# Performance work log

Hardware: AMD Instinct MI355X
Metric: run time of the kernel (lower is better)

## Reference

```python
import jax, jax.numpy as jnp
import numpy as np

IMG = 224
RADIUS_CUTS, AZIMUTH_CUTS = 16, 64
N_RADIUS, N_AZIMUTH = 25, 16          # kr1*kr2 = 25, ka^2 = 16
N_R = RADIUS_CUTS * N_RADIUS          # 400 sampled radii
N_A = AZIMUTH_CUTS * N_AZIMUTH        # 1024 sampled azimuths
EMBED_DIM = 96
KR, KA = 5, 4


def sample_grid(dist, H, W):
    """Per-batch polar sampling coordinates for the spherical distortion model.
    dist: (B, 4) polynomial distortion coefficients (module does dist.transpose(1,0)).
    Returns grid (B, N_R, N_A, 2) in grid_sample convention (x=width coord first),
    and theta_max (B,).
    """
    B = dist.shape[0]
    cf = 0.2 + dist.T                      # (4, B), positive odd-poly coefficients
    c = cf[:, :, None]                     # (4, B, 1) for broadcasting
    theta_max = jnp.full((B,), jnp.pi / 2, dtype=dist.dtype)

    def poly(t):                           # odd polynomial r(theta), t: (B, n)
        t2 = t * t
        return t * (c[0] + t2 * (c[1] + t2 * (c[2] + t2 * c[3])))

    # midpoint theta samples in (0, theta_max)
    theta = theta_max[:, None] * (jnp.arange(N_R, dtype=dist.dtype) + 0.5) / N_R  # (B, N_R)
    r = poly(theta) / poly(theta_max[:, None]) * (H * 0.5)                        # (B, N_R) pixels from center

    phi = (2.0 * jnp.pi) * (jnp.arange(N_A, dtype=dist.dtype) + 0.5) / N_A        # (N_A,)
    xc = r[:, :, None] * jnp.cos(phi)      # (B, N_R, N_A)
    yc = r[:, :, None] * jnp.sin(phi)
    # module: out = cat((yc/(W//2), xc/(H//2)), dim=3)
    grid = jnp.stack([yc / (W // 2), xc / (H // 2)], axis=-1)
    return grid, theta_max


def grid_sample_bilinear(img, grid):
    """torch.nn.functional.grid_sample, bilinear, align_corners=True, zeros padding.
    img: (B,C,H,W), grid: (B,Ho,Wo,2) with grid[...,0]=x (width), grid[...,1]=y (height).
    """
    B, C, H, W = img.shape
    gx = (grid[..., 0] + 1.0) * 0.5 * (W - 1)   # align_corners=True mapping
    gy = (grid[..., 1] + 1.0) * 0.5 * (H - 1)
    x0 = jnp.floor(gx); y0 = jnp.floor(gy)
    wx1 = gx - x0; wx0 = 1.0 - wx1
    wy1 = gy - y0; wy0 = 1.0 - wy1

    def corner(xi, yi, w):
        valid = (xi >= 0) & (xi <= W - 1) & (yi >= 0) & (yi <= H - 1)
        xc_ = jnp.clip(xi, 0, W - 1).astype(jnp.int32)
        yc_ = jnp.clip(yi, 0, H - 1).astype(jnp.int32)
        v = jax.vmap(lambda im, yy, xx: im[:, yy, xx])(img, yc_, xc_)  # (B,C,Ho,Wo)
        return v * (w * valid)[:, None, :, :]

    return (corner(x0, y0, wx0 * wy0) + corner(x0 + 1, y0, wx1 * wy0)
            + corner(x0, y0 + 1, wx0 * wy1) + corner(x0 + 1, y0 + 1, wx1 * wy1))


def conv2d(x, w, b, stride):
    y = jax.lax.conv_general_dilated(x, w, window_strides=stride, padding='VALID',
                                     dimension_numbers=('NCHW', 'OIHW', 'NCHW'))
    return y + b[None, :, None, None]


def setup_inputs() -> dict:
    key = jax.random.key(0)
    k = jax.random.split(key, 6)
    x = jax.random.uniform(k[0], (32, 3, IMG, IMG), dtype=jnp.float32)
    dist = jax.random.uniform(k[1], (32, 4), dtype=jnp.float32)
    w1 = jax.random.normal(k[2], (EMBED_DIM, 3, KR, KA), dtype=jnp.float32) * 0.05
    b1 = jnp.zeros((EMBED_DIM,), dtype=jnp.float32)
    w2 = jax.random.normal(k[3], (EMBED_DIM, EMBED_DIM, KR, KA), dtype=jnp.float32) * 0.05
    b2 = jnp.zeros((EMBED_DIM,), dtype=jnp.float32)
    return {"x": x, "dist": dist, "w1": w1, "b1": b1, "w2": w2, "b2": b2}


def reference(x, dist, w1, b1, w2, b2):
    B, C, H, W = x.shape
    grid, theta_max = sample_grid(dist, H, W)          # (B,400,1024,2)
    sampled = grid_sample_bilinear(x, grid)            # (B,3,400,1024)
    t = conv2d(sampled, w1, b1, (KR, KA))              # (B,96,80,256)
    t = conv2d(t, w2, b2, (KR, KA))                    # (B,96,16,64)
    t = t.reshape(B, EMBED_DIM, -1).transpose(0, 2, 1) # (B,1024,96)
    return (t, theta_max)
```

## Files before the change

kernel.cpp:

```cpp
#include <hip/hip_runtime.h>
#include <hip/hip_bf16.h>
#include <math.h>

#define NBATCH 32
#define IMGSZ  224
#define NR     400
#define NA     1024
#define ED     96
#define SROW   266

typedef __attribute__((ext_vector_type(8))) __bf16 bf16x8;
typedef __attribute__((ext_vector_type(8), aligned(8))) __bf16 bf16x8u;
typedef __attribute__((ext_vector_type(4), aligned(8))) __bf16 bf16x4a;
typedef __attribute__((ext_vector_type(4))) __bf16 bf16x4;
typedef __attribute__((ext_vector_type(4))) float f32x4;

union frag_u { struct { bf16x4a lo, hi; } p; bf16x8 v; };


#define PACK_N   (NBATCH*IMGSZ*IMGSZ)
#define PACK_N4  (PACK_N/4)
#define PACK_B   ((PACK_N4 + 255)/256)
#define PREP_N   (ED*ED*20 + 12*64*8 + NBATCH*NR + NA + NBATCH)
#define PREP_B   ((PREP_N + 255)/256)

__global__ __launch_bounds__(256)
void prep_pack_kernel(const float* __restrict__ x,
                      const float* __restrict__ dist,
                      const float* __restrict__ w1,
                      const float* __restrict__ w2,
                      __bf16* __restrict__ xp,
                      float* __restrict__ rtab,
                      float* __restrict__ costab,
                      float* __restrict__ sintab,
                      __bf16* __restrict__ w2f,
                      __bf16* __restrict__ w1f,
                      float* __restrict__ theta_out) {
    const float PI = 3.14159265358979323846f;
    const float SC = 223.0f / 224.0f;
    int bid = blockIdx.x;

    if (bid < PACK_B) {
        int i4 = bid*256 + threadIdx.x;
        if (i4 >= PACK_N4) return;
        int idx = i4 * 4;
        int b  = idx / (IMGSZ*IMGSZ);
        int px = idx - b*(IMGSZ*IMGSZ);
        const float* p = x + (size_t)b*3*IMGSZ*IMGSZ + px;
        f32x4 cr = *(const f32x4*)(p);
        f32x4 cg = *(const f32x4*)(p + IMGSZ*IMGSZ);
        f32x4 cb = *(const f32x4*)(p + 2*IMGSZ*IMGSZ);
        bf16x8 o0, o1;
        o0[0] = (__bf16)cr[0]; o0[1] = (__bf16)cg[0]; o0[2] = (__bf16)cb[0]; o0[3] = (__bf16)0.0f;
        o0[4] = (__bf16)cr[1]; o0[5] = (__bf16)cg[1]; o0[6] = (__bf16)cb[1]; o0[7] = (__bf16)0.0f;
        o1[0] = (__bf16)cr[2]; o1[1] = (__bf16)cg[2]; o1[2] = (__bf16)cb[2]; o1[3] = (__bf16)0.0f;
        o1[4] = (__bf16)cr[3]; o1[5] = (__bf16)cg[3]; o1[6] = (__bf16)cb[3]; o1[7] = (__bf16)0.0f;
        *(bf16x8*)(xp + (size_t)idx*4)     = o0;
        *(bf16x8*)(xp + (size_t)idx*4 + 8) = o1;
        return;
    }

    int idx = (bid - PACK_B)*256 + threadIdx.x;
    if (idx < ED*ED*20) {
        int j    = idx & 7;
        int lane = (idx >> 3) & 63;
        int grp  = idx >> 9;
        int nt   = grp % 6;
        int t    = grp / 6;
        int icb  = t % 3;
        int p    = t / 3;
        int sw   = (((p & 3) + icb) & 1) * 4;
        int oc = nt*16 + (lane & 15);
        int ic = icb*32 + (lane >> 4)*8 + (j ^ sw);
        w2f[idx] = (__bf16)w2[((size_t)(oc*ED + ic)*5 + (p >> 2))*4 + (p & 3)];
    } else if (idx < ED*ED*20 + 12*64*8) {
        int i2   = idx - ED*ED*20;
        int j    = i2 & 7;
        int lane = (i2 >> 3) & 63;
        int grp  = i2 >> 9;
        int ks = grp / 6, ot = grp % 6;
        int oc = ot*16 + (lane & 15);
        int k  = ks*32 + (lane >> 4)*8 + j;
        w1f[i2] = (k < 60) ? (__bf16)w1[oc*60 + k] : (__bf16)0.0f;
    } else if (idx < ED*ED*20 + 12*64*8 + NBATCH*NR) {
        int i2 = idx - ED*ED*20 - 12*64*8;
        int b = i2 / NR, i = i2 % NR;
        float c0 = 0.2f + dist[b*4+0];
        float c1 = 0.2f + dist[b*4+1];
        float c2 = 0.2f + dist[b*4+2];
        float c3 = 0.2f + dist[b*4+3];
        float tmax = 0.5f * PI;
        float t  = tmax * ((float)i + 0.5f) / (float)NR;
        float t2 = t * t;
        float pt = t * (c0 + t2*(c1 + t2*(c2 + t2*c3)));
        float tm2 = tmax * tmax;
        float pm = tmax * (c0 + tm2*(c1 + tm2*(c2 + tm2*c3)));
        rtab[i2] = pt / pm * (0.5f * (float)IMGSZ);
    } else if (idx < ED*ED*20 + 12*64*8 + NBATCH*NR + NA) {
        int j = idx - ED*ED*20 - 12*64*8 - NBATCH*NR;
        float phi = 2.0f * PI * ((float)j + 0.5f) / (float)NA;
        costab[j] = cosf(phi) * SC;
        sintab[j] = sinf(phi) * SC;
    } else if (idx < PREP_N) {
        theta_out[idx - (ED*ED*20 + 12*64*8 + NBATCH*NR + NA)] = 0.5f * PI;
    }
}

__global__ __launch_bounds__(256, 4)
void mega_kernel(const __bf16* __restrict__ xp,
                 const __bf16* __restrict__ w1f_g,
                 const __bf16* __restrict__ w2f,
                 const float* __restrict__ b1,
                 const float* __restrict__ b2,
                 const float* __restrict__ rtab,
                 const float* __restrict__ costab,
                 const float* __restrict__ sintab,
                 float* __restrict__ out) {
    __shared__ __attribute__((aligned(16))) char smem[32576];
    __bf16* s_samp = (__bf16*)smem;
    __bf16* t1f    = (__bf16*)(smem + 8000);
    __bf16* s_w1f  = (__bf16*)(smem + 20288);
    float*  red    = (float*)smem;

    int tid = threadIdx.x;
    int bid = blockIdx.x;
    int r2h = bid & 7;
    int aq  = (bid >> 3) & 3;
    int b   = bid >> 5;
    int wave = tid >> 6, lane = tid & 63, l15 = lane & 15, quad = lane >> 4;

    #pragma unroll
    for (int i = 0; i < 3; ++i)
        *(bf16x8*)(s_w1f + i*2048 + tid*8) = *(const bf16x8*)(w1f_g + i*2048 + tid*8);

    int az = aq*256 + tid;
    float sn = sintab[az];
    float cs = costab[az];
    const __bf16* xpb = xp + (size_t)b*IMGSZ*IMGSZ*4;
    const float* rb;

    auto sample = [&](int kr) {
        #pragma unroll
        for (int q = 0; q < 5; ++q) {
            float r  = rb[kr*5 + q];
            float gx = fmaf(r, sn, 111.5f);
            float gy = fmaf(r, cs, 111.5f);
            float x0f = floorf(gx), y0f = floorf(gy);
            float wx1 = gx - x0f, wx0 = 1.0f - wx1;
            float wy1 = gy - y0f, wy0 = 1.0f - wy1;
            int ix = (int)x0f, iy = (int)y0f;
            ix = min(max(ix, 0), IMGSZ-2);
            iy = min(max(iy, 0), IMGSZ-2);
            const __bf16* img = xpb + ((size_t)iy*IMGSZ + ix)*4;
            bf16x8u p0 = *(const bf16x8u*)img;
            bf16x8u p1 = *(const bf16x8u*)(img + IMGSZ*4);
            float w00 = wy0*wx0, w01 = wy0*wx1, w10 = wy1*wx0, w11 = wy1*wx1;
            #pragma unroll
            for (int c = 0; c < 3; ++c) {
                float v = w00*(float)p0[c] + w01*(float)p0[4+c]
                        + w10*(float)p1[c] + w11*(float)p1[4+c];
                s_samp[(c*5 + q)*SROW + tid] = (__bf16)v;
            }
        }
    };

    #pragma unroll 1
    for (int u = 0; u < 2; ++u) {
        int r2 = r2h*2 + u;
        rb = rtab + b*NR + r2*25;

        if (u) __syncthreads();

        f32x4 acc2[6];
        #pragma unroll
        for (int nt = 0; nt < 6; ++nt) acc2[nt] = (f32x4){0.f,0.f,0.f,0.f};

        sample(0);

        for (int kr = 0; kr < 5; ++kr) {
            __syncthreads();

            int colb = (wave*16 + l15)*4;
            f32x4 acc1[6];
            #pragma unroll
            for (int ot = 0; ot < 6; ++ot) acc1[ot] = (f32x4){0.f,0.f,0.f,0.f};

            frag_u fa, fb;
            fa.p.lo = *(const bf16x4a*)&s_samp[(quad*2    )*SROW + colb];
            fa.p.hi = *(const bf16x4a*)&s_samp[(quad*2 + 1)*SROW + colb];
            fb.p.lo = *(const bf16x4a*)&s_samp[(8 + quad*2)*SROW + colb];
            if (quad == 3) fb.p.hi = (bf16x4a){};
            else           fb.p.hi = *(const bf16x4a*)&s_samp[(9 + quad*2)*SROW + colb];

            #pragma unroll
            for (int ot = 0; ot < 6; ++ot) {
                bf16x8 wf0 = *(const bf16x8*)(s_w1f + (ot     )*512 + lane*8);
                bf16x8 wf1 = *(const bf16x8*)(s_w1f + (6 + ot )*512 + lane*8);
                acc1[ot] = __builtin_amdgcn_mfma_f32_16x16x32_bf16(wf0, fa.v, acc1[ot], 0, 0, 0);
                acc1[ot] = __builtin_amdgcn_mfma_f32_16x16x32_bf16(wf1, fb.v, acc1[ot], 0, 0, 0);
            }

            int pixel = wave*16 + l15;
            int a2l = pixel >> 2, ka = pixel & 3;
            #pragma unroll
            for (int ot = 0; ot < 6; ++ot) {
                f32x4 v = acc1[ot] + *(const f32x4*)(b1 + ot*16 + quad*4);
                bf16x4a wv;
                wv[0] = (__bf16)v[0]; wv[1] = (__bf16)v[1];
                wv[2] = (__bf16)v[2]; wv[3] = (__bf16)v[3];
                int icbase = ot*16 + quad*4;
                int kk = ka*3 + (icbase >> 5);
                int qT = (icbase >> 3) & 3;
                int jb = (icbase & 7) ^ ((kk & 1)*4);
                *(bf16x4a*)&t1f[((kk*4 + qT)*16 + a2l)*8 + jb] = wv;
            }
            __syncthreads();

            #pragma unroll
            for (int icb = 0; icb < 3; ++icb) {
                int kk = wave*3 + icb;
                int p  = kr*4 + wave;
                bf16x8 af = *(const bf16x8*)&t1f[(kk*64 + lane)*8];
                const __bf16* wp = w2f + (size_t)((p*3 + icb)*6)*512 + lane*8;
                #pragma unroll
                for (int nt = 0; nt < 6; ++nt) {
                    bf16x8 bf = *(const bf16x8*)(wp + nt*512);
                    acc2[nt] = __builtin_amdgcn_mfma_f32_16x16x32_bf16(af, bf, acc2[nt], 0, 0, 0);
                }
            }

            __builtin_amdgcn_sched_barrier(0);

            if (kr < 4) sample(kr + 1);
        }

        __syncthreads();
        if (wave) {
            float* rw = red + (wave - 1)*1568;
            #pragma unroll
            for (int nt = 0; nt < 6; ++nt)
                #pragma unroll
                for (int r = 0; r < 4; ++r)
                    rw[(quad*4 + r)*98 + nt*16 + l15] = acc2[nt][r];
        }
        __syncthreads();
        if (wave == 0) {
            size_t ob = ((size_t)b*1024 + r2*64 + aq*16)*ED;
            #pragma unroll
            for (int nt = 0; nt < 6; ++nt) {
                int oc = nt*16 + l15;
                float bias = b2[oc];
                #pragma unroll
                for (int r = 0; r < 4; ++r) {
                    int row = quad*4 + r;
                    float v = acc2[nt][r] + bias
                            + red[row*98 + oc]
                            + red[1568 + row*98 + oc]
                            + red[3136 + row*98 + oc];
                    out[ob + (size_t)row*ED + oc] = v;
                }
            }
        }
    }
}

extern "C" void kernel_launch(void* const* d_in, const int* in_sizes, int n_in,
                              void* d_out, int out_size, void* d_ws, size_t ws_size,
                              hipStream_t stream) {
    const float* x    = (const float*)d_in[0];
    const float* dist = (const float*)d_in[1];
    const float* w1   = (const float*)d_in[2];
    const float* b1   = (const float*)d_in[3];
    const float* w2   = (const float*)d_in[4];
    const float* b2   = (const float*)d_in[5];
    float* out = (float*)d_out;

    float* rtab   = (float*)d_ws;
    float* costab = rtab + NBATCH*NR;
    float* sintab = costab + NA;
    __bf16* w2f   = (__bf16*)(sintab + NA);
    __bf16* w1f   = w2f + ED*ED*20;
    __bf16* xp    = w1f + 12*64*8;

    float* theta_out = out + (size_t)NBATCH*1024*ED;

    prep_pack_kernel<<<PACK_B + PREP_B, 256, 0, stream>>>(
        x, dist, w1, w2, xp, rtab, costab, sintab, w2f, w1f, theta_out);
    mega_kernel<<<NBATCH*32, 256, 0, stream>>>(
        xp, w1f, w2f, b1, b2, rtab, costab, sintab, out);
}
```

Baseline: 165.0 us.

## Pack image rows with next-row pixels and split mega kernel per radius row

Adds an optional packed image layout in which each pixel holds its own RGB and the RGB of the pixel one row below. A bilinear tap then needs two adjacent 16-byte loads instead of two loads one row apart. This path is selected when the workspace is large enough, and it doubles the packed image size and prep write traffic. Separately, the mega kernel now handles one radius row per block instead of looping over two, doubling the grid to 2048 blocks. That raises parallelism but repeats the per-block w1 staging and sin/cos loads.

```diff
diff --git a/kernel.cpp b/kernel.cpp
--- a/kernel.cpp
+++ b/kernel.cpp
@@ -24,6 +24,7 @@
 #define PREP_N   (ED*ED*20 + 12*64*8 + NBATCH*NR + NA + NBATCH)
 #define PREP_B   ((PREP_N + 255)/256)
 
+template<bool RD>
 __global__ __launch_bounds__(256)
 void prep_pack_kernel(const float* __restrict__ x,
                       const float* __restrict__ dist,
@@ -44,19 +45,41 @@
         int i4 = bid*256 + threadIdx.x;
         if (i4 >= PACK_N4) return;
         int idx = i4 * 4;
-        int b  = idx / (IMGSZ*IMGSZ);
-        int px = idx - b*(IMGSZ*IMGSZ);
-        const float* p = x + (size_t)b*3*IMGSZ*IMGSZ + px;
-        f32x4 cr = *(const f32x4*)(p);
-        f32x4 cg = *(const f32x4*)(p + IMGSZ*IMGSZ);
-        f32x4 cb = *(const f32x4*)(p + 2*IMGSZ*IMGSZ);
-        bf16x8 o0, o1;
-        o0[0] = (__bf16)cr[0]; o0[1] = (__bf16)cg[0]; o0[2] = (__bf16)cb[0]; o0[3] = (__bf16)0.0f;
-        o0[4] = (__bf16)cr[1]; o0[5] = (__bf16)cg[1]; o0[6] = (__bf16)cb[1]; o0[7] = (__bf16)0.0f;
-        o1[0] = (__bf16)cr[2]; o1[1] = (__bf16)cg[2]; o1[2] = (__bf16)cb[2]; o1[3] = (__bf16)0.0f;
-        o1[4] = (__bf16)cr[3]; o1[5] = (__bf16)cg[3]; o1[6] = (__bf16)cb[3]; o1[7] = (__bf16)0.0f;
-        *(bf16x8*)(xp + (size_t)idx*4)     = o0;
-        *(bf16x8*)(xp + (size_t)idx*4 + 8) = o1;
+        int b   = idx / (IMGSZ*IMGSZ);
+        int rem = idx - b*(IMGSZ*IMGSZ);
+        const float* pl = x + (size_t)b*3*IMGSZ*IMGSZ;
+        if constexpr (RD) {
+            int y    = rem / IMGSZ;
+            int xcol = rem - y*IMGSZ;
+            int yn = min(y + 1, IMGSZ - 1);
+            f32x4 r0[3], r1[3];
+            #pragma unroll
+            for (int c = 0; c < 3; ++c) {
+                r0[c] = *(const f32x4*)(pl + (size_t)c*IMGSZ*IMGSZ + y *IMGSZ + xcol);
+                r1[c] = *(const f32x4*)(pl + (size_t)c*IMGSZ*IMGSZ + yn*IMGSZ + xcol);
+            }
+            #pragma unroll
+            for (int e = 0; e < 4; ++e) {
+                bf16x8 o;
+                o[0] = (__bf16)r0[0][e]; o[1] = (__bf16)r0[1][e];
+                o[2] = (__bf16)r0[2][e]; o[3] = (__bf16)0.0f;
+                o[4] = (__bf16)r1[0][e]; o[5] = (__bf16)r1[1][e];
+                o[6] = (__bf16)r1[2][e]; o[7] = (__bf16)0.0f;
+                *(bf16x8*)(xp + (size_t)(idx + e)*8) = o;
+            }
+        } else {
+            const float* p = pl + rem;
+            f32x4 cr = *(const f32x4*)(p);
+            f32x4 cg = *(const f32x4*)(p + IMGSZ*IMGSZ);
+            f32x4 cb = *(const f32x4*)(p + 2*IMGSZ*IMGSZ);
+            bf16x8 o0, o1;
+            o0[0] = (__bf16)cr[0]; o0[1] = (__bf16)cg[0]; o0[2] = (__bf16)cb[0]; o0[3] = (__bf16)0.0f;
+            o0[4] = (__bf16)cr[1]; o0[5] = (__bf16)cg[1]; o0[6] = (__bf16)cb[1]; o0[7] = (__bf16)0.0f;
+            o1[0] = (__bf16)cr[2]; o1[1] = (__bf16)cg[2]; o1[2] = (__bf16)cb[2]; o1[3] = (__bf16)0.0f;
+            o1[4] = (__bf16)cr[3]; o1[5] = (__bf16)cg[3]; o1[6] = (__bf16)cb[3]; o1[7] = (__bf16)0.0f;
+            *(bf16x8*)(xp + (size_t)idx*4)     = o0;
+            *(bf16x8*)(xp + (size_t)idx*4 + 8) = o1;
+        }
         return;
     }
 
@@ -106,6 +129,7 @@
     }
 }
 
+template<bool RD>
 __global__ __launch_bounds__(256, 4)
 void mega_kernel(const __bf16* __restrict__ xp,
                  const __bf16* __restrict__ w1f_g,
@@ -124,9 +148,9 @@
 
     int tid = threadIdx.x;
     int bid = blockIdx.x;
-    int r2h = bid & 7;
-    int aq  = (bid >> 3) & 3;
-    int b   = bid >> 5;
+    int r2 = bid & 15;
+    int aq = (bid >> 4) & 3;
+    int b  = bid >> 6;
     int wave = tid >> 6, lane = tid & 63, l15 = lane & 15, quad = lane >> 4;
 
     #pragma unroll
@@ -136,8 +160,12 @@
     int az = aq*256 + tid;
     float sn = sintab[az];
     float cs = costab[az];
-    const __bf16* xpb = xp + (size_t)b*IMGSZ*IMGSZ*4;
-    const float* rb;
+    const __bf16* xpb = xp + (size_t)b*IMGSZ*IMGSZ*(RD ? 8 : 4);
+    const float* rb = rtab + b*NR + r2*25;
+
+    f32x4 acc2[6];
+    #pragma unroll
+    for (int nt = 0; nt < 6; ++nt) acc2[nt] = (f32x4){0.f,0.f,0.f,0.f};
 
     auto sample = [&](int kr) {
         #pragma unroll
@@ -151,114 +179,114 @@
             int ix = (int)x0f, iy = (int)y0f;
             ix = min(max(ix, 0), IMGSZ-2);
             iy = min(max(iy, 0), IMGSZ-2);
-            const __bf16* img = xpb + ((size_t)iy*IMGSZ + ix)*4;
-            bf16x8u p0 = *(const bf16x8u*)img;
-            bf16x8u p1 = *(const bf16x8u*)(img + IMGSZ*4);
             float w00 = wy0*wx0, w01 = wy0*wx1, w10 = wy1*wx0, w11 = wy1*wx1;
-            #pragma unroll
-            for (int c = 0; c < 3; ++c) {
-                float v = w00*(float)p0[c] + w01*(float)p0[4+c]
-                        + w10*(float)p1[c] + w11*(float)p1[4+c];
-                s_samp[(c*5 + q)*SROW + tid] = (__bf16)v;
+            if constexpr (RD) {
+                const __bf16* img = xpb + ((size_t)iy*IMGSZ + ix)*8;
+                bf16x8u p0 = *(const bf16x8u*)img;
+                bf16x8u p1 = *(const bf16x8u*)(img + 8);
+                #pragma unroll
+                for (int c = 0; c < 3; ++c) {
+                    float v = w00*(float)p0[c]   + w01*(float)p1[c]
+                            + w10*(float)p0[4+c] + w11*(float)p1[4+c];
+                    s_samp[(c*5 + q)*SROW + tid] = (__bf16)v;
+                }
+            } else {
+                const __bf16* img = xpb + ((size_t)iy*IMGSZ + ix)*4;
+                bf16x8u p0 = *(const bf16x8u*)img;
+                bf16x8u p1 = *(const bf16x8u*)(img + IMGSZ*4);
+                #pragma unroll
+                for (int c = 0; c < 3; ++c) {
+                    float v = w00*(float)p0[c] + w01*(float)p0[4+c]
+                            + w10*(float)p1[c] + w11*(float)p1[4+c];
+                    s_samp[(c*5 + q)*SROW + tid] = (__bf16)v;
+                }
             }
         }
     };
 
-    #pragma unroll 1
-    for (int u = 0; u < 2; ++u) {
-        int r2 = r2h*2 + u;
-        rb = rtab + b*NR + r2*25;
-
-        if (u) __syncthreads();
-
-        f32x4 acc2[6];
-        #pragma unroll
-        for (int nt = 0; nt < 6; ++nt) acc2[nt] = (f32x4){0.f,0.f,0.f,0.f};
-
-        sample(0);
-
-        for (int kr = 0; kr < 5; ++kr) {
-            __syncthreads();
-
-            int colb = (wave*16 + l15)*4;
-            f32x4 acc1[6];
-            #pragma unroll
-            for (int ot = 0; ot < 6; ++ot) acc1[ot] = (f32x4){0.f,0.f,0.f,0.f};
-
-            frag_u fa, fb;
-            fa.p.lo = *(const bf16x4a*)&s_samp[(quad*2    )*SROW + colb];
-            fa.p.hi = *(const bf16x4a*)&s_samp[(quad*2 + 1)*SROW + colb];
-            fb.p.lo = *(const bf16x4a*)&s_samp[(8 + quad*2)*SROW + colb];
-            if (quad == 3) fb.p.hi = (bf16x4a){};
-            else           fb.p.hi = *(const bf16x4a*)&s_samp[(9 + quad*2)*SROW + colb];
-
-            #pragma unroll
-            for (int ot = 0; ot < 6; ++ot) {
-                bf16x8 wf0 = *(const bf16x8*)(s_w1f + (ot     )*512 + lane*8);
-                bf16x8 wf1 = *(const bf16x8*)(s_w1f + (6 + ot )*512 + lane*8);
-                acc1[ot] = __builtin_amdgcn_mfma_f32_16x16x32_bf16(wf0, fa.v, acc1[ot], 0, 0, 0);
-                acc1[ot] = __builtin_amdgcn_mfma_f32_16x16x32_bf16(wf1, fb.v, acc1[ot], 0, 0, 0);
-            }
-
-            int pixel = wave*16 + l15;
-            int a2l = pixel >> 2, ka = pixel & 3;
-            #pragma unroll
-            for (int ot = 0; ot < 6; ++ot) {
-                f32x4 v = acc1[ot] + *(const f32x4*)(b1 + ot*16 + quad*4);
-                bf16x4a wv;
-                wv[0] = (__bf16)v[0]; wv[1] = (__bf16)v[1];
-                wv[2] = (__bf16)v[2]; wv[3] = (__bf16)v[3];
-                int icbase = ot*16 + quad*4;
-                int kk = ka*3 + (icbase >> 5);
-                int qT = (icbase >> 3) & 3;
-                int jb = (icbase & 7) ^ ((kk & 1)*4);
-                *(bf16x4a*)&t1f[((kk*4 + qT)*16 + a2l)*8 + jb] = wv;
-            }
-            __syncthreads();
-
-            #pragma unroll
-            for (int icb = 0; icb < 3; ++icb) {
-                int kk = wave*3 + icb;
-                int p  = kr*4 + wave;
-                bf16x8 af = *(const bf16x8*)&t1f[(kk*64 + lane)*8];
-                const __bf16* wp = w2f + (size_t)((p*3 + icb)*6)*512 + lane*8;
-                #pragma unroll
-                for (int nt = 0; nt < 6; ++nt) {
-                    bf16x8 bf = *(const bf16x8*)(wp + nt*512);
-                    acc2[nt] = __builtin_amdgcn_mfma_f32_16x16x32_bf16(af, bf, acc2[nt], 0, 0, 0);
-                }
-            }
-
-            __builtin_amdgcn_sched_barrier(0);
-
-            if (kr < 4) sample(kr + 1);
-        }
-
+    sample(0);
+
+    for (int kr = 0; kr < 5; ++kr) {
         __syncthreads();
-        if (wave) {
-            float* rw = red + (wave - 1)*1568;
-            #pragma unroll
-            for (int nt = 0; nt < 6; ++nt)
-                #pragma unroll
-                for (int r = 0; r < 4; ++r)
-                    rw[(quad*4 + r)*98 + nt*16 + l15] = acc2[nt][r];
+
+        int colb = (wave*16 + l15)*4;
+        f32x4 acc1[6];
+        #pragma unroll
+        for (int ot = 0; ot < 6; ++ot) acc1[ot] = (f32x4){0.f,0.f,0.f,0.f};
+
+        frag_u fa, fb;
+        fa.p.lo = *(const bf16x4a*)&s_samp[(quad*2    )*SROW + colb];
+        fa.p.hi = *(const bf16x4a*)&s_samp[(quad*2 + 1)*SROW + colb];
+        fb.p.lo = *(const bf16x4a*)&s_samp[(8 + quad*2)*SROW + colb];
+        if (quad == 3) fb.p.hi = (bf16x4a){};
+        else           fb.p.hi = *(const bf16x4a*)&s_samp[(9 + quad*2)*SROW + colb];
+
+        #pragma unroll
+        for (int ot = 0; ot < 6; ++ot) {
+            bf16x8 wf0 = *(const bf16x8*)(s_w1f + (ot     )*512 + lane*8);
+            bf16x8 wf1 = *(const bf16x8*)(s_w1f + (6 + ot )*512 + lane*8);
+            acc1[ot] = __builtin_amdgcn_mfma_f32_16x16x32_bf16(wf0, fa.v, acc1[ot], 0, 0, 0);
+            acc1[ot] = __builtin_amdgcn_mfma_f32_16x16x32_bf16(wf1, fb.v, acc1[ot], 0, 0, 0);
+        }
+
+        int pixel = wave*16 + l15;
+        int a2l = pixel >> 2, ka = pixel & 3;
+        #pragma unroll
+        for (int ot = 0; ot < 6; ++ot) {
+            f32x4 v = acc1[ot] + *(const f32x4*)(b1 + ot*16 + quad*4);
+            bf16x4a wv;
+            wv[0] = (__bf16)v[0]; wv[1] = (__bf16)v[1];
+            wv[2] = (__bf16)v[2]; wv[3] = (__bf16)v[3];
+            int icbase = ot*16 + quad*4;
+            int kk = ka*3 + (icbase >> 5);
+            int qT = (icbase >> 3) & 3;
+            int jb = (icbase & 7) ^ ((kk & 1)*4);
+            *(bf16x4a*)&t1f[((kk*4 + qT)*16 + a2l)*8 + jb] = wv;
         }
         __syncthreads();
-        if (wave == 0) {
-            size_t ob = ((size_t)b*1024 + r2*64 + aq*16)*ED;
+
+        #pragma unroll
+        for (int icb = 0; icb < 3; ++icb) {
+            int kk = wave*3 + icb;
+            int p  = kr*4 + wave;
+            bf16x8 af = *(const bf16x8*)&t1f[(kk*64 + lane)*8];
+            const __bf16* wp = w2f + (size_t)((p*3 + icb)*6)*512 + lane*8;
             #pragma unroll
             for (int nt = 0; nt < 6; ++nt) {
-                int oc = nt*16 + l15;
-                float bias = b2[oc];
-                #pragma unroll
-                for (int r = 0; r < 4; ++r) {
-                    int row = quad*4 + r;
-                    float v = acc2[nt][r] + bias
-                            + red[row*98 + oc]
-                            + red[1568 + row*98 + oc]
-                            + red[3136 + row*98 + oc];
-                    out[ob + (size_t)row*ED + oc] = v;
-                }
+                bf16x8 bf = *(const bf16x8*)(wp + nt*512);
+                acc2[nt] = __builtin_amdgcn_mfma_f32_16x16x32_bf16(af, bf, acc2[nt], 0, 0, 0);
+            }
+        }
+
+        __builtin_amdgcn_sched_barrier(0);
+
+        if (kr < 4) sample(kr + 1);
+    }
+
+    __syncthreads();
+    if (wave) {
+        float* rw = red + (wave - 1)*1568;
+        #pragma unroll
+        for (int nt = 0; nt < 6; ++nt)
+            #pragma unroll
+            for (int r = 0; r < 4; ++r)
+                rw[(quad*4 + r)*98 + nt*16 + l15] = acc2[nt][r];
+    }
+    __syncthreads();
+    if (wave == 0) {
+        size_t ob = ((size_t)b*1024 + r2*64 + aq*16)*ED;
+        #pragma unroll
+        for (int nt = 0; nt < 6; ++nt) {
+            int oc = nt*16 + l15;
+            float bias = b2[oc];
+            #pragma unroll
+            for (int r = 0; r < 4; ++r) {
+                int row = quad*4 + r;
+                float v = acc2[nt][r] + bias
+                        + red[row*98 + oc]
+                        + red[1568 + row*98 + oc]
+                        + red[3136 + row*98 + oc];
+                out[ob + (size_t)row*ED + oc] = v;
             }
         }
     }
@@ -284,8 +312,17 @@
 
     float* theta_out = out + (size_t)NBATCH*1024*ED;
 
-    prep_pack_kernel<<<PACK_B + PREP_B, 256, 0, stream>>>(
-        x, dist, w1, w2, xp, rtab, costab, sintab, w2f, w1f, theta_out);
-    mega_kernel<<<NBATCH*32, 256, 0, stream>>>(
-        xp, w1f, w2f, b1, b2, rtab, costab, sintab, out);
+    bool rd = ws_size >= (size_t)27000000;
+
+    if (rd) {
+        prep_pack_kernel<true><<<PACK_B + PREP_B, 256, 0, stream>>>(
+            x, dist, w1, w2, xp, rtab, costab, sintab, w2f, w1f, theta_out);
+        mega_kernel<true><<<NBATCH*16*4, 256, 0, stream>>>(
+            xp, w1f, w2f, b1, b2, rtab, costab, sintab, out);
+    } else {
+        prep_pack_kernel<false><<<PACK_B + PREP_B, 256, 0, stream>>>(
+            x, dist, w1, w2, xp, rtab, costab, sintab, w2f, w1f, theta_out);
+        mega_kernel<false><<<NBATCH*16*4, 256, 0, stream>>>(
+            xp, w1f, w2f, b1, b2, rtab, costab, sintab, out);
+    }
 }
```

New measurement: 145.8 us. 1.13x faster.
